# Performance work log

Measured on AMD Instinct MI355X. Metric: run time of the kernel, lower is better.

Reference implementation:

```python
import jax, jax.numpy as jnp
import numpy as np

B_SZ, T, I, N = 32, 128, 16, 512
DT = 0.01          # dt inside mem_update_ahs / output neuron
TAU_M, TAU_ADP = 64.0, 32.0
B_J0, BETA_AD = 0.04, 1.8
B_INIT = 0.1       # default b in mem_update_ahs
R_M = 1.0
B_DECAYED = 0.08
# surrogate-gradient constants (module globals)
SG_ALPHA, SG_BETA, SG_GAMMA = 0.4, 0.5, 0.5


@jax.custom_vjp
def act_fun(x):
    # spike = (x > 0).float() with surrogate gradient
    return (x > 0).astype(x.dtype)

def _act_fwd(x):
    return act_fun(x), x

def _act_bwd(x, g):
    # tanh(alpha * exp(-x^2)**beta) * gamma,  beta=0.5 -> exp(-x^2/2)
    temp = jnp.tanh(SG_ALPHA * jnp.exp(-SG_BETA * x * x))
    return (g * temp * SG_GAMMA,)

act_fun.defvjp(_act_fwd, _act_bwd)


def setup_inputs() -> dict:
    key = jax.random.key(0)
    ks = jax.random.split(key, 14)
    std = 0.02
    d = {"x": jax.random.normal(ks[0], (B_SZ, T, I), jnp.float32)}
    names = ["U_j", "U_i", "U_f", "U_o", "W_j", "W_i", "W_f", "W_o",
             "b_j", "b_i", "b_f", "b_o"]
    shapes = [(I, 1, N)] * 4 + [(I, N, N)] * 4 + [(I, N)] * 4
    for i, (n, s) in enumerate(zip(names, shapes)):
        d[n] = jax.random.normal(ks[i + 1], s, jnp.float32) * std
    return d


def _es_lstm(x, U_j, U_i, U_f, U_o, W_j, W_i, W_f, W_o, b_j, b_i, b_f, b_o):
    B = x.shape[0]
    h0 = jnp.zeros((B, I, N), x.dtype)
    c0 = jnp.zeros((B, I, N), x.dtype)

    a_out = jnp.exp(jnp.float32(-DT))  # output neuron leak, tau_m = 1

    def step(carry, x_t):
        h, c = carry  # [B, I, N]; x_t: [B, I]

        def gate(W, U, b, act):
            # recurrent: per-channel matmul; input: rank-1 broadcast of x_t with U
            return act(jnp.einsum('bin,ink->bik', h, W)
                       + x_t[:, :, None] * U[:, 0, :] + b)

        j = gate(W_j, U_j, b_j, jnp.tanh)
        i = gate(W_i, U_i, b_i, jax.nn.sigmoid)
        f = gate(W_f, U_f, b_f, jax.nn.sigmoid)
        o = gate(W_o, U_o, b_o, jax.nn.sigmoid)

        # mem_update_ahs(inputs=h, mem=j, spike=i)
        alpha_m = jnp.exp(-(DT / TAU_M) * 0.5 * j)
        ro = jnp.exp(-(DT / TAU_ADP) * 0.5 * i)
        b_ad = ro * B_INIT + (1.0 - ro) * i
        Bth = B_J0 + BETA_AD * b_ad
        mem = j * alpha_m + (1.0 - alpha_m) * R_M * h - Bth * i * DT
        spike = act_fun(mem - Bth)

        # output_SpikeNeuron(inputs=spike, mem=mem, tau_m=1)
        mem_out = mem * a_out + (1.0 - a_out) * R_M * spike + B_DECAYED

        c_new = c * f + i * spike * mem_out
        h_new = o * jnp.tanh(c_new)
        return (h_new, c_new), h_new

    (h_fin, c_fin), outs = jax.lax.scan(step, (h0, c0), jnp.swapaxes(x, 0, 1))
    outputs = jnp.swapaxes(outs, 0, 1)  # [B, T, I, N]
    return outputs, h_fin, c_fin


def reference(x, U_j, U_i, U_f, U_o, W_j, W_i, W_f, W_o, b_j, b_i, b_f, b_o):
    return _es_lstm(x, U_j, U_i, U_f, U_o, W_j, W_i, W_f, W_o,
                    b_j, b_i, b_f, b_o)
```

## Files before the change

### kernel.cpp

```cpp
#include <hip/hip_runtime.h>
#include <hip/hip_bf16.h>

typedef __hip_bfloat16 bf16;
typedef unsigned short ushort_t;
typedef __attribute__((ext_vector_type(8))) short short8;
typedef __attribute__((ext_vector_type(4))) float float4v;

#define BSZ 32
#define TT  128
#define IC  16
#define NDIM 512
#define WS_NEED ((size_t)4 * IC * NDIM * NDIM * 2)
#define SMEM_BYTES 131072

__device__ __attribute__((aligned(256))) unsigned g_flag[IC * 64];
__device__ __attribute__((aligned(256))) ushort_t g_hx[2][IC][BSZ * NDIM];

__device__ __forceinline__ unsigned f2bfb(float f) {
    bf16 h = __float2bfloat16(f);
    return (unsigned)*reinterpret_cast<unsigned short*>(&h);
}
__device__ __forceinline__ float frcp(float x) { return __builtin_amdgcn_rcpf(x); }
__device__ __forceinline__ float ftanh(float x) {
    float cx = fminf(fmaxf(x, -9.0f), 9.0f);
    float e  = __expf(2.0f * cx);
    return 1.0f - 2.0f * frcp(e + 1.0f);
}
__device__ __forceinline__ float fsig(float x) {
    return frcp(1.0f + __expf(-x));
}
__device__ __forceinline__ float sigf(float v) { return 1.0f / (1.0f + expf(-v)); }

__global__ void pack_w(const float* __restrict__ Wj, const float* __restrict__ Wi,
                       const float* __restrict__ Wf, const float* __restrict__ Wo,
                       uint4* __restrict__ wpk)
{
    __shared__ float tile[NDIM][17];
    const int blk  = blockIdx.x;
    if (blk == 0) {
        for (int k = threadIdx.x; k < IC * 64; k += 256) g_flag[k] = 0u;
    }
    const int nt16 = blk & 31;
    const int i    = (blk >> 5) & 15;
    const int g    = blk >> 9;
    const float* W = (g == 0) ? Wj : (g == 1) ? Wi : (g == 2) ? Wf : Wo;
    const float* base = W + (size_t)i * NDIM * NDIM + nt16 * 16;
    const int tid = threadIdx.x;

    #pragma unroll
    for (int r = 0; r < 2; r++) {
        int n = tid + r * 256;
        const float4* p = (const float4*)(base + (size_t)n * NDIM);
        float4 v0 = p[0], v1 = p[1], v2 = p[2], v3 = p[3];
        float* d = &tile[n][0];
        d[0]=v0.x; d[1]=v0.y; d[2]=v0.z; d[3]=v0.w;
        d[4]=v1.x; d[5]=v1.y; d[6]=v1.z; d[7]=v1.w;
        d[8]=v2.x; d[9]=v2.y; d[10]=v2.z; d[11]=v2.w;
        d[12]=v3.x; d[13]=v3.y; d[14]=v3.z; d[15]=v3.w;
    }
    __syncthreads();
    #pragma unroll
    for (int p = 0; p < 4; p++) {
        int f = p * 256 + tid;
        int kstep = f >> 6, L = f & 63;
        int quad = L >> 4, col = L & 15;
        int nr = kstep * 32 + quad * 8;
        unsigned u[4];
        #pragma unroll
        for (int w = 0; w < 4; w++) {
            unsigned lo = f2bfb(tile[nr + 2 * w][col]);
            unsigned hi = f2bfb(tile[nr + 2 * w + 1][col]);
            u[w] = lo | (hi << 16);
        }
        wpk[(size_t)blk * 1024 + (size_t)kstep * 64 + L] = make_uint4(u[0], u[1], u[2], u[3]);
    }
}

__launch_bounds__(256, 1)
__global__ void es_persist(
    const float* __restrict__ x,
    const float* __restrict__ Uj, const float* __restrict__ Ui,
    const float* __restrict__ Uf, const float* __restrict__ Uo,
    const uint4* __restrict__ wpk,
    const float* __restrict__ bj, const float* __restrict__ bi,
    const float* __restrict__ bfp, const float* __restrict__ bo,
    float* __restrict__ out)
{
    extern __shared__ unsigned char smem[];
    unsigned char* h_base = smem;

    const int bid = blockIdx.x;
    const int i   = bid & 15;
    const int kt  = bid >> 4;
    const int tid = threadIdx.x;
    const int wid = tid >> 6, L = tid & 63;
    const int quad = L >> 4, c15 = L & 15;
    const int ntl  = wid & 1;
    const int nt16 = kt * 2 + ntl;
    const int Mh   = (wid >> 1) * 16;

    float* hfin = out + (size_t)BSZ * TT * IC * NDIM;
    float* cfin = hfin + (size_t)BSZ * IC * NDIM;

    const size_t gstride = (size_t)IC * 32 * 1024;
    const uint4* bbase = wpk + ((size_t)i * 32 + nt16) * 1024 + L;
    short8 bfr0[16], bfr1[16], bfr2[16], bfr3[16];
    #pragma unroll
    for (int ks = 0; ks < 16; ks++) bfr0[ks] = *(const short8*)(bbase + (size_t)ks * 64);
    #pragma unroll
    for (int ks = 0; ks < 16; ks++) bfr1[ks] = *(const short8*)(bbase + gstride + (size_t)ks * 64);
    #pragma unroll
    for (int ks = 0; ks < 16; ks++) bfr2[ks] = *(const short8*)(bbase + 2 * gstride + (size_t)ks * 64);
    #pragma unroll
    for (int ks = 0; ks < 16; ks++) bfr3[ks] = *(const short8*)(bbase + 3 * gstride + (size_t)ks * 64);

    const int n = nt16 * 16 + c15;
    const size_t un = (size_t)i * NDIM + n;
    const float u0 = Uj[un], u1 = Ui[un], u2 = Uf[un], u3 = Uo[un];
    const float c0 = bj[un], c1 = bi[un], c2 = bfp[un], c3 = bo[un];
    const float a_out = 0.990049834f;
    const float onea  = 0.009950166f;

    float cc[4] = {0.f, 0.f, 0.f, 0.f};

    #pragma unroll 1
    for (int t = 0; t < TT; t++) {
        float4v acc0 = {0,0,0,0}, acc1 = {0,0,0,0}, acc2 = {0,0,0,0}, acc3 = {0,0,0,0};

        float xv[4];
        #pragma unroll
        for (int r = 0; r < 4; r++)
            xv[r] = x[(size_t)((Mh + quad * 4 + r) * TT + t) * IC + i];

        if (t > 0) {
            {
                const unsigned* fp = &g_flag[(i << 6) + (L & 15)];
                bool need = (L < 16);
                unsigned v = 0;
                int spins = 0;
                while (__ballot((int)need) != 0ull) {
                    if (need) {
                        asm volatile("global_load_dword %0, %1, off sc0 sc1\n\ts_waitcnt vmcnt(0)"
                                     : "=v"(v) : "v"(fp) : "memory");
                        if (v >= (unsigned)t) need = false;
                    }
                    if (need && spins > 8) __builtin_amdgcn_s_sleep(1);
                    if (++spins > 40000) break;
                }
            }

            const ushort_t* gsrc = &g_hx[(t - 1) & 1][i][0];
            float4v hg[8];
            #pragma unroll
            for (int q = 0; q < 8; q++) {
                const ushort_t* s = gsrc + (size_t)(q * 4 + wid) * NDIM + L * 8;
                asm volatile("global_load_dwordx4 %0, %1, off sc0 sc1" : "=v"(hg[q]) : "v"(s));
            }
            asm volatile("s_waitcnt vmcnt(0)" ::: "memory");
            __builtin_amdgcn_sched_barrier(0);

            #pragma unroll
            for (int q = 0; q < 8; q++) {
                int b = q * 4 + wid;
                *(float4v*)(h_base + b * 1024 + ((L ^ (b & 7)) << 4)) = hg[q];
            }
            __syncthreads();

            const int arow = Mh + c15;
            const unsigned char* aptr = h_base + arow * 1024;
            const int ax = arow & 7;
            #pragma unroll
            for (int ks = 0; ks < 16; ks++) {
                short8 a = *(const short8*)(aptr + (((ks * 4 + quad) ^ ax) << 4));
                acc0 = __builtin_amdgcn_mfma_f32_16x16x32_bf16(a, bfr0[ks], acc0, 0, 0, 0);
                acc1 = __builtin_amdgcn_mfma_f32_16x16x32_bf16(a, bfr1[ks], acc1, 0, 0, 0);
                acc2 = __builtin_amdgcn_mfma_f32_16x16x32_bf16(a, bfr2[ks], acc2, 0, 0, 0);
                acc3 = __builtin_amdgcn_mfma_f32_16x16x32_bf16(a, bfr3[ks], acc3, 0, 0, 0);
            }
        }

        ushort_t* gdst = &g_hx[t & 1][i][0];
        #pragma unroll
        for (int r = 0; r < 4; r++) {
            const int b = Mh + quad * 4 + r;

            float jg = ftanh(acc0[r] + c0 + xv[r] * u0);
            float ig = fsig (acc1[r] + c1 + xv[r] * u1);
            float fg = fsig (acc2[r] + c2 + xv[r] * u2);
            float og = fsig (acc3[r] + c3 + xv[r] * u3);

            float am1 = 7.8125e-5f * jg;
            float s1  = 1.5625e-4f * ig;
            float b_ad = fmaf(s1, ig - 0.1f, 0.1f);
            float Bth  = fmaf(1.8f, b_ad, 0.04f);

            float hprev = 0.0f;
            if (t > 0)
                hprev = __bfloat162float(*(const bf16*)(h_base + b * 1024
                            + (((n >> 3) ^ (b & 7)) << 4) + (n & 7) * 2));

            float mem   = fmaf(am1, hprev - jg, jg) - 0.01f * Bth * ig;
            float spike = (mem - Bth) > 0.0f ? 1.0f : 0.0f;
            float mem_o = mem * a_out + onea * spike + 0.08f;

            float cn = fmaf(cc[r], fg, ig * spike * mem_o);
            float hn = og * ftanh(cn);
            cc[r] = cn;

            ushort_t* gp = gdst + (size_t)b * NDIM + n;
            unsigned hb = f2bfb(hn);
            asm volatile("global_store_short %0, %1, off sc0 sc1" :: "v"(gp), "v"(hb) : "memory");
            out[((size_t)(b * TT + t) * IC + i) * NDIM + n] = hn;
            if (t == TT - 1) {
                size_t sidx = ((size_t)b * IC + i) * NDIM + n;
                cfin[sidx] = cn;
                hfin[sidx] = hn;
            }
        }

        if (t < TT - 1) {
            asm volatile("s_waitcnt vmcnt(0)" ::: "memory");
            __syncthreads();
            if (tid == 0) {
                unsigned tv = (unsigned)(t + 1);
                const unsigned* fp = &g_flag[(i << 6) + kt];
                asm volatile("global_store_dword %0, %1, off sc0 sc1" :: "v"(fp), "v"(tv) : "memory");
            }
        }
    }
}

#define KT 32
#define NC 64
__launch_bounds__(256)
__global__ void step_kernel_valu(int t,
    const float* __restrict__ x,
    const float* __restrict__ Uj, const float* __restrict__ Ui, const float* __restrict__ Uf, const float* __restrict__ Uo,
    const float* __restrict__ Wj, const float* __restrict__ Wi, const float* __restrict__ Wf, const float* __restrict__ Wo,
    const float* __restrict__ bj, const float* __restrict__ bi, const float* __restrict__ bfp, const float* __restrict__ bo,
    float* __restrict__ out)
{
    __shared__ float w_lds[NC][KT * 4 + 4];
    __shared__ float h_lds[NC][BSZ + 4];
    const int i = blockIdx.x, k0 = blockIdx.y * KT, tid = threadIdx.x;
    const int kl = tid & 31, bg = tid >> 5, kg = k0 + kl;
    float* hfin = out + (size_t)BSZ * TT * IC * NDIM;
    float* cfin = hfin + (size_t)BSZ * IC * NDIM;
    float acc[4][4];
    {
        size_t uidx = (size_t)i * NDIM + kg;
        float u0 = Uj[uidx], u1 = Ui[uidx], u2 = Uf[uidx], u3 = Uo[uidx];
        float c0 = bj[uidx], c1 = bi[uidx], c2 = bfp[uidx], c3 = bo[uidx];
        #pragma unroll
        for (int j = 0; j < 4; j++) {
            int b = bg * 4 + j;
            float xv = x[(size_t)(b * TT + t) * IC + i];
            acc[0][j] = c0 + xv * u0; acc[1][j] = c1 + xv * u1;
            acc[2][j] = c2 + xv * u2; acc[3][j] = c3 + xv * u3;
        }
    }
    if (t > 0) {
        for (int n0 = 0; n0 < NDIM; n0 += NC) {
            __syncthreads();
            {
                int g = tid >> 6, nn = tid & 63;
                const float* Wp = (g == 0) ? Wj : (g == 1) ? Wi : (g == 2) ? Wf : Wo;
                const float4* p = (const float4*)(Wp + ((size_t)i * NDIM + (size_t)(n0 + nn)) * NDIM + k0);
                #pragma unroll
                for (int q = 0; q < 8; q++) {
                    float4 v = p[q];
                    w_lds[nn][(q * 4 + 0) * 4 + g] = v.x; w_lds[nn][(q * 4 + 1) * 4 + g] = v.y;
                    w_lds[nn][(q * 4 + 2) * 4 + g] = v.z; w_lds[nn][(q * 4 + 3) * 4 + g] = v.w;
                }
            }
            {
                int b = tid >> 3, nb = (tid & 7) * 8;
                const float4* ph = (const float4*)(out + ((size_t)(b * TT + (t - 1)) * IC + i) * NDIM + n0 + nb);
                float4 h0 = ph[0], h1 = ph[1];
                h_lds[nb + 0][b] = h0.x; h_lds[nb + 1][b] = h0.y; h_lds[nb + 2][b] = h0.z; h_lds[nb + 3][b] = h0.w;
                h_lds[nb + 4][b] = h1.x; h_lds[nb + 5][b] = h1.y; h_lds[nb + 6][b] = h1.z; h_lds[nb + 7][b] = h1.w;
            }
            __syncthreads();
            #pragma unroll 8
            for (int nn = 0; nn < NC; nn++) {
                float4 wv = *(const float4*)&w_lds[nn][kl * 4];
                float4 hv = *(const float4*)&h_lds[nn][bg * 4];
                acc[0][0] += hv.x * wv.x; acc[1][0] += hv.x * wv.y; acc[2][0] += hv.x * wv.z; acc[3][0] += hv.x * wv.w;
                acc[0][1] += hv.y * wv.x; acc[1][1] += hv.y * wv.y; acc[2][1] += hv.y * wv.z; acc[3][1] += hv.y * wv.w;
                acc[0][2] += hv.z * wv.x; acc[1][2] += hv.z * wv.y; acc[2][2] += hv.z * wv.z; acc[3][2] += hv.z * wv.w;
                acc[0][3] += hv.w * wv.x; acc[1][3] += hv.w * wv.y; acc[2][3] += hv.w * wv.z; acc[3][3] += hv.w * wv.w;
            }
        }
    }
    const float a_out = 0.990049834f;
    #pragma unroll
    for (int j = 0; j < 4; j++) {
        int b = bg * 4 + j;
        size_t sidx = ((size_t)b * IC + i) * NDIM + kg;
        float jg = tanhf(acc[0][j]), ig = sigf(acc[1][j]), fg = sigf(acc[2][j]), og = sigf(acc[3][j]);
        float alpha_m = expf(-7.8125e-5f * jg);
        float ro = expf(-1.5625e-4f * ig);
        float b_ad = ro * 0.1f + (1.0f - ro) * ig;
        float Bth = 0.04f + 1.8f * b_ad;
        float hprev = 0.0f, cprev = 0.0f;
        if (t > 0) { hprev = out[((size_t)(b * TT + (t - 1)) * IC + i) * NDIM + kg]; cprev = cfin[sidx]; }
        float mem = jg * alpha_m + (1.0f - alpha_m) * hprev - Bth * ig * 0.01f;
        float spike = (mem - Bth) > 0.0f ? 1.0f : 0.0f;
        float mem_o = mem * a_out + (1.0f - a_out) * spike + 0.08f;
        float cn = cprev * fg + ig * spike * mem_o;
        float hn = og * tanhf(cn);
        cfin[sidx] = cn;
        out[((size_t)(b * TT + t) * IC + i) * NDIM + kg] = hn;
        if (t == TT - 1) hfin[sidx] = hn;
    }
}

extern "C" void kernel_launch(void* const* d_in, const int* in_sizes, int n_in,
                              void* d_out, int out_size, void* d_ws, size_t ws_size,
                              hipStream_t stream) {
    const float* x   = (const float*)d_in[0];
    const float* Uj  = (const float*)d_in[1];
    const float* Ui_ = (const float*)d_in[2];
    const float* Uf  = (const float*)d_in[3];
    const float* Uo  = (const float*)d_in[4];
    const float* Wj  = (const float*)d_in[5];
    const float* Wi  = (const float*)d_in[6];
    const float* Wf  = (const float*)d_in[7];
    const float* Wo  = (const float*)d_in[8];
    const float* bj  = (const float*)d_in[9];
    const float* bi_ = (const float*)d_in[10];
    const float* bf_ = (const float*)d_in[11];
    const float* bo  = (const float*)d_in[12];
    float* out = (float*)d_out;

    if (ws_size >= WS_NEED) {
        static bool attr_set = false;
        if (!attr_set) {
            (void)hipFuncSetAttribute((const void*)es_persist,
                                      hipFuncAttributeMaxDynamicSharedMemorySize, SMEM_BYTES);
            attr_set = true;
        }
        pack_w<<<dim3(2048), dim3(256), 0, stream>>>(Wj, Wi, Wf, Wo, (uint4*)d_ws);
        es_persist<<<dim3(256), dim3(256), SMEM_BYTES, stream>>>(
            x, Uj, Ui_, Uf, Uo, (const uint4*)d_ws, bj, bi_, bf_, bo, out);
    } else {
        for (int t = 0; t < TT; t++) {
            step_kernel_valu<<<dim3(IC, NDIM / KT), dim3(256), 0, stream>>>(
                t, x, Uj, Ui_, Uf, Uo, Wj, Wi, Wf, Wo, bj, bi_, bf_, bo, out);
        }
    }
}
```

Measured before the change: 699.3 us.

## Split persistent LSTM across 512 blocks with per-gate waves and LDS exchange

The persistent kernel now launches 512 blocks, two per CU, instead of 256. Each block owns a 16-column tile for one channel, and each wave computes one gate's recurrent matmul over both 16-row batch halves. The gate pre-activations go through a padded LDS buffer so every thread can finish the elementwise update for two adjacent columns. That update packs the two bf16 h values into a single dword store. The aim is to spread the MFMA and register load over more CUs and raise occupancy. The costs are an extra barrier and an LDS round trip per step, plus twice as many blocks to synchronise through the global flags (32 per channel).

```diff
diff --git a/kernel.cpp b/kernel.cpp
--- a/kernel.cpp
+++ b/kernel.cpp
@@ -11,7 +11,7 @@
 #define IC  16
 #define NDIM 512
 #define WS_NEED ((size_t)4 * IC * NDIM * NDIM * 2)
-#define SMEM_BYTES 131072
+#define SMEM_BYTES (32768 + 4 * 32 * 17 * 4)
 
 __device__ __attribute__((aligned(256))) unsigned g_flag[IC * 64];
 __device__ __attribute__((aligned(256))) ushort_t g_hx[2][IC][BSZ * NDIM];
@@ -76,7 +76,7 @@
     }
 }
 
-__launch_bounds__(256, 1)
+__launch_bounds__(256, 2)
 __global__ void es_persist(
     const float* __restrict__ x,
     const float* __restrict__ Uj, const float* __restrict__ Ui,
@@ -88,54 +88,49 @@
 {
     extern __shared__ unsigned char smem[];
     unsigned char* h_base = smem;
+    float* pre_lds = (float*)(smem + 32768);
 
     const int bid = blockIdx.x;
-    const int i   = bid & 15;
-    const int kt  = bid >> 4;
+    const int low = bid & 255;
+    const int i   = (low >> 5) | ((bid >> 8) << 3);
+    const int kt  = bid & 31;
     const int tid = threadIdx.x;
     const int wid = tid >> 6, L = tid & 63;
     const int quad = L >> 4, c15 = L & 15;
-    const int ntl  = wid & 1;
-    const int nt16 = kt * 2 + ntl;
-    const int Mh   = (wid >> 1) * 16;
 
     float* hfin = out + (size_t)BSZ * TT * IC * NDIM;
     float* cfin = hfin + (size_t)BSZ * IC * NDIM;
 
-    const size_t gstride = (size_t)IC * 32 * 1024;
-    const uint4* bbase = wpk + ((size_t)i * 32 + nt16) * 1024 + L;
-    short8 bfr0[16], bfr1[16], bfr2[16], bfr3[16];
+    const uint4* bbase = wpk + (((size_t)wid * IC + i) * 32 + kt) * 1024 + L;
+    short8 bfr[16];
     #pragma unroll
-    for (int ks = 0; ks < 16; ks++) bfr0[ks] = *(const short8*)(bbase + (size_t)ks * 64);
-    #pragma unroll
-    for (int ks = 0; ks < 16; ks++) bfr1[ks] = *(const short8*)(bbase + gstride + (size_t)ks * 64);
-    #pragma unroll
-    for (int ks = 0; ks < 16; ks++) bfr2[ks] = *(const short8*)(bbase + 2 * gstride + (size_t)ks * 64);
-    #pragma unroll
-    for (int ks = 0; ks < 16; ks++) bfr3[ks] = *(const short8*)(bbase + 3 * gstride + (size_t)ks * 64);
-
-    const int n = nt16 * 16 + c15;
-    const size_t un = (size_t)i * NDIM + n;
-    const float u0 = Uj[un], u1 = Ui[un], u2 = Uf[un], u3 = Uo[un];
-    const float c0 = bj[un], c1 = bi[un], c2 = bfp[un], c3 = bo[un];
+    for (int ks = 0; ks < 16; ks++) bfr[ks] = *(const short8*)(bbase + (size_t)ks * 64);
+
+    const int eb  = tid >> 3;
+    const int en0 = (tid & 7) * 2;
+    const int n0  = kt * 16 + en0;
+    const size_t un = (size_t)i * NDIM + n0;
+    const float uja = Uj[un], ujb = Uj[un + 1];
+    const float uia = Ui[un], uib = Ui[un + 1];
+    const float ufa = Uf[un], ufb = Uf[un + 1];
+    const float uoa = Uo[un], uob = Uo[un + 1];
+    const float cja = bj[un], cjb = bj[un + 1];
+    const float cia = bi[un], cib = bi[un + 1];
+    const float cfa = bfp[un], cfb = bfp[un + 1];
+    const float coa = bo[un], cob = bo[un + 1];
     const float a_out = 0.990049834f;
     const float onea  = 0.009950166f;
 
-    float cc[4] = {0.f, 0.f, 0.f, 0.f};
+    float cc0 = 0.0f, cc1 = 0.0f;
 
     #pragma unroll 1
     for (int t = 0; t < TT; t++) {
-        float4v acc0 = {0,0,0,0}, acc1 = {0,0,0,0}, acc2 = {0,0,0,0}, acc3 = {0,0,0,0};
-
-        float xv[4];
-        #pragma unroll
-        for (int r = 0; r < 4; r++)
-            xv[r] = x[(size_t)((Mh + quad * 4 + r) * TT + t) * IC + i];
+        float xv = x[(size_t)(eb * TT + t) * IC + i];
 
         if (t > 0) {
             {
-                const unsigned* fp = &g_flag[(i << 6) + (L & 15)];
-                bool need = (L < 16);
+                const unsigned* fp = &g_flag[(i << 6) + (L & 31)];
+                bool need = (L < 32);
                 unsigned v = 0;
                 int spins = 0;
                 while (__ballot((int)need) != 0ull) {
@@ -166,56 +161,85 @@
             }
             __syncthreads();
 
-            const int arow = Mh + c15;
-            const unsigned char* aptr = h_base + arow * 1024;
-            const int ax = arow & 7;
             #pragma unroll
-            for (int ks = 0; ks < 16; ks++) {
-                short8 a = *(const short8*)(aptr + (((ks * 4 + quad) ^ ax) << 4));
-                acc0 = __builtin_amdgcn_mfma_f32_16x16x32_bf16(a, bfr0[ks], acc0, 0, 0, 0);
-                acc1 = __builtin_amdgcn_mfma_f32_16x16x32_bf16(a, bfr1[ks], acc1, 0, 0, 0);
-                acc2 = __builtin_amdgcn_mfma_f32_16x16x32_bf16(a, bfr2[ks], acc2, 0, 0, 0);
-                acc3 = __builtin_amdgcn_mfma_f32_16x16x32_bf16(a, bfr3[ks], acc3, 0, 0, 0);
-            }
-        }
-
-        ushort_t* gdst = &g_hx[t & 1][i][0];
+            for (int mh = 0; mh < 2; mh++) {
+                const int arow = mh * 16 + c15;
+                const unsigned char* aptr = h_base + arow * 1024;
+                const int ax = arow & 7;
+                float4v acc = {0, 0, 0, 0};
+                #pragma unroll
+                for (int ks = 0; ks < 16; ks++) {
+                    short8 a = *(const short8*)(aptr + (((ks * 4 + quad) ^ ax) << 4));
+                    acc = __builtin_amdgcn_mfma_f32_16x16x32_bf16(a, bfr[ks], acc, 0, 0, 0);
+                }
+                #pragma unroll
+                for (int r = 0; r < 4; r++)
+                    pre_lds[wid * 544 + (mh * 16 + quad * 4 + r) * 17 + c15] = acc[r];
+            }
+            __syncthreads();
+        }
+
+        float p0[4], p1[4];
         #pragma unroll
-        for (int r = 0; r < 4; r++) {
-            const int b = Mh + quad * 4 + r;
-
-            float jg = ftanh(acc0[r] + c0 + xv[r] * u0);
-            float ig = fsig (acc1[r] + c1 + xv[r] * u1);
-            float fg = fsig (acc2[r] + c2 + xv[r] * u2);
-            float og = fsig (acc3[r] + c3 + xv[r] * u3);
-
+        for (int g = 0; g < 4; g++) {
+            p0[g] = (t > 0) ? pre_lds[g * 544 + eb * 17 + en0]     : 0.0f;
+            p1[g] = (t > 0) ? pre_lds[g * 544 + eb * 17 + en0 + 1] : 0.0f;
+        }
+        float hprev0 = 0.0f, hprev1 = 0.0f;
+        if (t > 0) {
+            hprev0 = __bfloat162float(*(const bf16*)(h_base + eb * 1024
+                        + ((((n0)     >> 3) ^ (eb & 7)) << 4) + ((n0)     & 7) * 2));
+            hprev1 = __bfloat162float(*(const bf16*)(h_base + eb * 1024
+                        + ((((n0 + 1) >> 3) ^ (eb & 7)) << 4) + ((n0 + 1) & 7) * 2));
+        }
+
+        float hn0, hn1;
+        {
+            float jg = ftanh(p0[0] + cja + xv * uja);
+            float ig = fsig (p0[1] + cia + xv * uia);
+            float fg = fsig (p0[2] + cfa + xv * ufa);
+            float og = fsig (p0[3] + coa + xv * uoa);
             float am1 = 7.8125e-5f * jg;
             float s1  = 1.5625e-4f * ig;
             float b_ad = fmaf(s1, ig - 0.1f, 0.1f);
             float Bth  = fmaf(1.8f, b_ad, 0.04f);
-
-            float hprev = 0.0f;
-            if (t > 0)
-                hprev = __bfloat162float(*(const bf16*)(h_base + b * 1024
-                            + (((n >> 3) ^ (b & 7)) << 4) + (n & 7) * 2));
-
-            float mem   = fmaf(am1, hprev - jg, jg) - 0.01f * Bth * ig;
+            float mem   = fmaf(am1, hprev0 - jg, jg) - 0.01f * Bth * ig;
             float spike = (mem - Bth) > 0.0f ? 1.0f : 0.0f;
             float mem_o = mem * a_out + onea * spike + 0.08f;
-
-            float cn = fmaf(cc[r], fg, ig * spike * mem_o);
-            float hn = og * ftanh(cn);
-            cc[r] = cn;
-
-            ushort_t* gp = gdst + (size_t)b * NDIM + n;
-            unsigned hb = f2bfb(hn);
-            asm volatile("global_store_short %0, %1, off sc0 sc1" :: "v"(gp), "v"(hb) : "memory");
-            out[((size_t)(b * TT + t) * IC + i) * NDIM + n] = hn;
-            if (t == TT - 1) {
-                size_t sidx = ((size_t)b * IC + i) * NDIM + n;
-                cfin[sidx] = cn;
-                hfin[sidx] = hn;
-            }
+            float cn = fmaf(cc0, fg, ig * spike * mem_o);
+            hn0 = og * ftanh(cn);
+            cc0 = cn;
+        }
+        {
+            float jg = ftanh(p1[0] + cjb + xv * ujb);
+            float ig = fsig (p1[1] + cib + xv * uib);
+            float fg = fsig (p1[2] + cfb + xv * ufb);
+            float og = fsig (p1[3] + cob + xv * uob);
+            float am1 = 7.8125e-5f * jg;
+            float s1  = 1.5625e-4f * ig;
+            float b_ad = fmaf(s1, ig - 0.1f, 0.1f);
+            float Bth  = fmaf(1.8f, b_ad, 0.04f);
+            float mem   = fmaf(am1, hprev1 - jg, jg) - 0.01f * Bth * ig;
+            float spike = (mem - Bth) > 0.0f ? 1.0f : 0.0f;
+            float mem_o = mem * a_out + onea * spike + 0.08f;
+            float cn = fmaf(cc1, fg, ig * spike * mem_o);
+            hn1 = og * ftanh(cn);
+            cc1 = cn;
+        }
+
+        {
+            ushort_t* gp = &g_hx[t & 1][i][(size_t)eb * NDIM + n0];
+            unsigned hb = f2bfb(hn0) | (f2bfb(hn1) << 16);
+            asm volatile("global_store_dword %0, %1, off sc0 sc1" :: "v"(gp), "v"(hb) : "memory");
+        }
+        {
+            float* op = out + ((size_t)(eb * TT + t) * IC + i) * NDIM + n0;
+            op[0] = hn0; op[1] = hn1;
+        }
+        if (t == TT - 1) {
+            size_t sidx = ((size_t)eb * IC + i) * NDIM + n0;
+            cfin[sidx] = cc0; cfin[sidx + 1] = cc1;
+            hfin[sidx] = hn0; hfin[sidx + 1] = hn1;
         }
 
         if (t < TT - 1) {
@@ -341,7 +365,7 @@
             attr_set = true;
         }
         pack_w<<<dim3(2048), dim3(256), 0, stream>>>(Wj, Wi, Wf, Wo, (uint4*)d_ws);
-        es_persist<<<dim3(256), dim3(256), SMEM_BYTES, stream>>>(
+        es_persist<<<dim3(512), dim3(256), SMEM_BYTES, stream>>>(
             x, Uj, Ui_, Uf, Uo, (const uint4*)d_ws, bj, bi_, bf_, bo, out);
     } else {
         for (int t = 0; t < TT; t++) {
```

Measured after the change: 842.2 us. 20.4% more time.

## Stage h in LDS, publish with vector stores, defer output writes past flag

Applied to the files above, without the earlier changes.

Each block now gathers its new hidden-state tile into an LDS staging buffer and publishes it to the global exchange buffer with 16-byte stores, instead of scattered 2-byte stores. The exchange buffer layout is tiled per producer block, and the consumer's gather and swizzled LDS placement are rewritten to match. The fp32 output and final-state stores move after the flag release, so they no longer sit on the inter-block critical path. The spin loop also waits longer before sleeping. This adds an extra barrier per step and relies on the new layout matching on both the producer and consumer sides.

```diff
diff --git a/kernel.cpp b/kernel.cpp
--- a/kernel.cpp
+++ b/kernel.cpp
@@ -88,6 +88,7 @@
 {
     extern __shared__ unsigned char smem[];
     unsigned char* h_base = smem;
+    unsigned char* hx     = smem + 32768;
 
     const int bid = blockIdx.x;
     const int i   = bid & 15;
@@ -115,6 +116,7 @@
     for (int ks = 0; ks < 16; ks++) bfr3[ks] = *(const short8*)(bbase + 3 * gstride + (size_t)ks * 64);
 
     const int n = nt16 * 16 + c15;
+    const int nl = ntl * 16 + c15;
     const size_t un = (size_t)i * NDIM + n;
     const float u0 = Uj[un], u1 = Ui[un], u2 = Uf[un], u3 = Uo[un];
     const float c0 = bj[un], c1 = bi[un], c2 = bfp[un], c3 = bo[un];
@@ -122,6 +124,10 @@
     const float onea  = 0.009950166f;
 
     float cc[4] = {0.f, 0.f, 0.f, 0.f};
+
+    const int gb  = (tid >> 2) & 31;
+    const int gb7 = gb & 7;
+    const int tkb = (tid >> 7) * 4 + (tid & 3);
 
     #pragma unroll 1
     for (int t = 0; t < TT; t++) {
@@ -144,7 +150,7 @@
                                      : "=v"(v) : "v"(fp) : "memory");
                         if (v >= (unsigned)t) need = false;
                     }
-                    if (need && spins > 8) __builtin_amdgcn_s_sleep(1);
+                    if (need && spins > 64) __builtin_amdgcn_s_sleep(1);
                     if (++spins > 40000) break;
                 }
             }
@@ -152,17 +158,17 @@
             const ushort_t* gsrc = &g_hx[(t - 1) & 1][i][0];
             float4v hg[8];
             #pragma unroll
-            for (int q = 0; q < 8; q++) {
-                const ushort_t* s = gsrc + (size_t)(q * 4 + wid) * NDIM + L * 8;
-                asm volatile("global_load_dwordx4 %0, %1, off sc0 sc1" : "=v"(hg[q]) : "v"(s));
+            for (int l = 0; l < 8; l++) {
+                const ushort_t* s = gsrc + (size_t)l * 2048 + tid * 8;
+                asm volatile("global_load_dwordx4 %0, %1, off sc0 sc1" : "=v"(hg[l]) : "v"(s));
             }
             asm volatile("s_waitcnt vmcnt(0)" ::: "memory");
             __builtin_amdgcn_sched_barrier(0);
 
             #pragma unroll
-            for (int q = 0; q < 8; q++) {
-                int b = q * 4 + wid;
-                *(float4v*)(h_base + b * 1024 + ((L ^ (b & 7)) << 4)) = hg[q];
+            for (int l = 0; l < 8; l++) {
+                int cidx = l * 8 + tkb;
+                *(float4v*)(h_base + gb * 1024 + ((cidx ^ gb7) << 4)) = hg[l];
             }
             __syncthreads();
 
@@ -179,7 +185,7 @@
             }
         }
 
-        ushort_t* gdst = &g_hx[t & 1][i][0];
+        float hnv[4];
         #pragma unroll
         for (int r = 0; r < 4; r++) {
             const int b = Mh + quad * 4 + r;
@@ -205,26 +211,36 @@
 
             float cn = fmaf(cc[r], fg, ig * spike * mem_o);
             float hn = og * ftanh(cn);
-            cc[r] = cn;
-
-            ushort_t* gp = gdst + (size_t)b * NDIM + n;
-            unsigned hb = f2bfb(hn);
-            asm volatile("global_store_short %0, %1, off sc0 sc1" :: "v"(gp), "v"(hb) : "memory");
-            out[((size_t)(b * TT + t) * IC + i) * NDIM + n] = hn;
-            if (t == TT - 1) {
-                size_t sidx = ((size_t)b * IC + i) * NDIM + n;
-                cfin[sidx] = cn;
-                hfin[sidx] = hn;
-            }
+            cc[r] = cn; hnv[r] = hn;
+
+            *(ushort_t*)(hx + b * 80 + nl * 2) = (ushort_t)f2bfb(hn);
         }
 
         if (t < TT - 1) {
+            __syncthreads();
+            if (tid < 128) {
+                int row = tid >> 2, cg = tid & 3;
+                float4v v = *(const float4v*)(hx + row * 80 + cg * 16);
+                ushort_t* gp = &g_hx[t & 1][i][0] + kt * 1024 + row * 32 + cg * 8;
+                asm volatile("global_store_dwordx4 %0, %1, off sc0 sc1" :: "v"(gp), "v"(v) : "memory");
+            }
             asm volatile("s_waitcnt vmcnt(0)" ::: "memory");
             __syncthreads();
             if (tid == 0) {
                 unsigned tv = (unsigned)(t + 1);
                 const unsigned* fp = &g_flag[(i << 6) + kt];
                 asm volatile("global_store_dword %0, %1, off sc0 sc1" :: "v"(fp), "v"(tv) : "memory");
+            }
+        }
+
+        #pragma unroll
+        for (int r = 0; r < 4; r++) {
+            const int b = Mh + quad * 4 + r;
+            out[((size_t)(b * TT + t) * IC + i) * NDIM + n] = hnv[r];
+            if (t == TT - 1) {
+                size_t sidx = ((size_t)b * IC + i) * NDIM + n;
+                cfin[sidx] = cc[r];
+                hfin[sidx] = hnv[r];
             }
         }
     }
```

New measurement: 705.1 us. About the same (+0.8%).
